# Kernel optimization log

Measured on AMD Instinct MI355X. Metric: run time of the kernel, lower is better.

Reference implementation:

```python
import jax, jax.numpy as jnp
import numpy as np

N, E, F, H, G = 50000, 800000, 128, 256, 64


def _bn(x, p, eps=1e-3):
    # inference-mode BatchNormalization; p rows = [gamma, beta, moving_mean, moving_var]
    g, b, m, v = p
    return g * (x - m) * jax.lax.rsqrt(v + eps) + b


def _prelu(x, a):
    return jnp.where(x >= 0, x, a * x)


def _dense_bn_act(x, W, b, bn, a=None):
    h = _bn(x @ W + b, bn)
    return h if a is None else _prelu(h, a)


def _gconv(x, src, tgt, W, b, bn, a, n_nodes):
    # spektral GeneralConv: Dense -> BN -> PReLU -> propagate (gather sources, scatter-sum to targets)
    h = _prelu(_bn(x @ W + b, bn), a)
    return jax.ops.segment_sum(h[src], tgt, num_segments=n_nodes)


def setup_inputs():
    key = jax.random.key(0)
    ks = iter(jax.random.split(key, 64))

    def dense(i, o):
        W = jax.random.normal(next(ks), (i, o), jnp.float32) / np.float32(np.sqrt(i))
        b = 0.01 * jax.random.normal(next(ks), (o,), jnp.float32)
        return W, b

    def bn_p(c):
        k1, k2, k3, k4 = jax.random.split(next(ks), 4)
        return jnp.stack([
            1.0 + 0.1 * jax.random.normal(k1, (c,)),
            0.1 * jax.random.normal(k2, (c,)),
            0.1 * jax.random.normal(k3, (c,)),
            0.5 + jax.random.uniform(k4, (c,)),
        ]).astype(jnp.float32)

    inp = {}
    inp['x'] = jax.random.normal(next(ks), (N, F), jnp.float32)
    inp['edge_index'] = jax.random.randint(next(ks), (E, 2), 0, N, jnp.int32)
    inp['seg'] = jnp.sort(jax.random.randint(next(ks), (N,), 0, G, jnp.int32))
    inp['n_graphs'] = G
    dims = {'pre0': F, 'pre1': H, 'g0': H, 'g1': 2 * H, 'g2': 3 * H, 'g3': 4 * H, 'post0': 5 * H}
    for name, din in dims.items():
        W, b = dense(din, H)
        inp[name + '_W'], inp[name + '_b'] = W, b
        inp[name + '_bn'] = bn_p(H)
        inp[name + '_a'] = jnp.full((H,), 0.25, jnp.float32)
    W, b = dense(H, 1)
    inp['post1_W'], inp['post1_b'] = W, b
    inp['post1_bn'] = bn_p(1)
    return inp


def reference(x, edge_index, seg, n_graphs, pre0_W, pre0_b, pre0_bn, pre0_a, pre1_W, pre1_b, pre1_bn, pre1_a, g0_W, g0_b, g0_bn, g0_a, g1_W, g1_b, g1_bn, g1_a, g2_W, g2_b, g2_bn, g2_a, g3_W, g3_b, g3_bn, g3_a, post0_W, post0_b, post0_bn, post0_a, post1_W, post1_b, post1_bn):
    n_nodes = x.shape[0]
    tgt, src = edge_index[:, 0], edge_index[:, 1]
    # pre-process MLP (2 layers)
    out = _dense_bn_act(x, pre0_W, pre0_b, pre0_bn, pre0_a)
    out = _dense_bn_act(out, pre1_W, pre1_b, pre1_bn, pre1_a)
    # 4 message-passing layers with 'cat' skip connectivity
    for W, b, bn, a in ((g0_W, g0_b, g0_bn, g0_a), (g1_W, g1_b, g1_bn, g1_a), (g2_W, g2_b, g2_bn, g2_a), (g3_W, g3_b, g3_bn, g3_a)):
        z = _gconv(out, src, tgt, W, b, bn, a, n_nodes)
        out = jnp.concatenate([z, out], axis=-1)
    # post-process MLP: hidden layer (PReLU) then linear output layer (BN, no activation)
    out = _dense_bn_act(out, post0_W, post0_b, post0_bn, post0_a)
    out = _dense_bn_act(out, post1_W, post1_b, post1_bn)
    # global sum pool over nodes per graph -> [n_graphs, 1]
    return jax.ops.segment_sum(out, seg, num_segments=n_graphs)
```

## Files before the change

kernel.cpp:

```cpp
#include <hip/hip_runtime.h>
#include <hip/hip_bf16.h>

#define NN 50000
#define NEDGE 800000
#define HD 256
#define ACT_LD 1280
#define NGRAPH 64
#define BN_EPS 1e-3f

#define BM 128
#define BN 128
#define BK 64

#define SCAN_NBLK ((NN + 255) / 256)

using bf16 = __hip_bfloat16;
typedef __attribute__((ext_vector_type(8))) short bf16x8;
typedef __attribute__((ext_vector_type(4))) float f32x4;

#define GLB(p) ((const __attribute__((address_space(1))) void*)(p))
#define LDS(p) ((__attribute__((address_space(3))) void*)(p))

static __device__ __forceinline__ float bf2f(unsigned short u) {
    union { float f; unsigned int i; } c;
    c.i = ((unsigned int)u) << 16;
    return c.f;
}
static __device__ __forceinline__ unsigned short f2bf(float f) {
    bf16 t = __float2bfloat16(f);
    return *reinterpret_cast<unsigned short*>(&t);
}

__global__ __launch_bounds__(256)
void transpose_w(const float* __restrict__ W, bf16* __restrict__ Wt, int K)
{
    __shared__ unsigned short T[32][33];
    const int k0 = blockIdx.x * 32;
    const int n0 = blockIdx.y * 32;
#pragma unroll
    for (int i = 0; i < 4; ++i) {
        const int idx = threadIdx.x + i * 256;
        const int kk = idx >> 5, nn = idx & 31;
        T[kk][nn] = f2bf(W[(size_t)(k0 + kk) * HD + n0 + nn]);
    }
    __syncthreads();
#pragma unroll
    for (int i = 0; i < 4; ++i) {
        const int idx = threadIdx.x + i * 256;
        const int nn = idx >> 5, kk = idx & 31;
        unsigned short v = T[kk][nn];
        Wt[(size_t)(n0 + nn) * K + k0 + kk] = *reinterpret_cast<bf16*>(&v);
    }
}

__global__ __launch_bounds__(256)
void convert_x(const float* __restrict__ x, bf16* __restrict__ xb)
{
    const int i = blockIdx.x * blockDim.x + threadIdx.x;
    if (i >= NN * 32) return;
    const float4 v = *reinterpret_cast<const float4*>(x + (size_t)i * 4);
    ushort4 o;
    o.x = f2bf(v.x); o.y = f2bf(v.y); o.z = f2bf(v.z); o.w = f2bf(v.w);
    *reinterpret_cast<ushort4*>((unsigned short*)xb + (size_t)i * 4) = o;
}

__global__ __launch_bounds__(256)
void gemm_bn_act(const bf16* __restrict__ A, int lda,
                 const bf16* __restrict__ Wt, int K,
                 const float* __restrict__ bias,
                 const float* __restrict__ bn,
                 const float* __restrict__ alpha,
                 bf16* __restrict__ out, int ldo, int M)
{
    __shared__ short As[BM * BK];
    __shared__ short Bs[BN * BK];

    const int tid  = threadIdx.x;
    const int wid  = tid >> 6;
    const int lane = tid & 63;
    const int lo   = lane & 15;
    const int hi   = lane >> 4;
    const int wr   = wid >> 1;
    const int wc   = wid & 1;

    const int m0 = blockIdx.x * BM;
    const int n0 = blockIdx.y * BN;

    const int srow = lane >> 3;
    const int sel  = (lane & 7) * 8;

    f32x4 acc[4][4] = {};

    for (int k0 = 0; k0 < K; k0 += BK) {
        __syncthreads();
#pragma unroll
        for (int i = 0; i < 4; ++i) {
            const int grp = wid * 4 + i;
            const int row = grp * 8 + srow;
            const int ar  = (m0 + row < M) ? (m0 + row) : (M - 1);
            __builtin_amdgcn_global_load_lds(GLB(A + (size_t)ar * lda + k0 + sel),
                                             LDS(&As[grp * 8 * BK]), 16, 0, 0);
            __builtin_amdgcn_global_load_lds(GLB(Wt + (size_t)(n0 + row) * K + k0 + sel),
                                             LDS(&Bs[grp * 8 * BK]), 16, 0, 0);
        }
        __syncthreads();

#pragma unroll
        for (int kc = 0; kc < 2; ++kc) {
            bf16x8 af[4], bfr[4];
#pragma unroll
            for (int rt = 0; rt < 4; ++rt)
                af[rt] = *reinterpret_cast<const bf16x8*>(&As[(wr * 64 + rt * 16 + lo) * BK + kc * 32 + hi * 8]);
#pragma unroll
            for (int ct = 0; ct < 4; ++ct)
                bfr[ct] = *reinterpret_cast<const bf16x8*>(&Bs[(wc * 64 + ct * 16 + lo) * BK + kc * 32 + hi * 8]);
#pragma unroll
            for (int rt = 0; rt < 4; ++rt)
#pragma unroll
                for (int ct = 0; ct < 4; ++ct)
                    acc[rt][ct] = __builtin_amdgcn_mfma_f32_16x16x32_bf16(af[rt], bfr[ct], acc[rt][ct], 0, 0, 0);
        }
    }

    float sc[4], sh[4], al[4];
#pragma unroll
    for (int ct = 0; ct < 4; ++ct) {
        const int c = n0 + wc * 64 + ct * 16 + lo;
        const float g  = bn[c];
        const float be = bn[HD + c];
        const float mu = bn[2 * HD + c];
        const float va = bn[3 * HD + c];
        sc[ct] = g * rsqrtf(va + BN_EPS);
        sh[ct] = be + (bias[c] - mu) * sc[ct];
        al[ct] = alpha ? alpha[c] : 1.0f;
    }
#pragma unroll
    for (int rt = 0; rt < 4; ++rt) {
#pragma unroll
        for (int i = 0; i < 4; ++i) {
            const int r = m0 + wr * 64 + rt * 16 + hi * 4 + i;
            if (r >= M) continue;
#pragma unroll
            for (int ct = 0; ct < 4; ++ct) {
                float v = acc[rt][ct][i] * sc[ct] + sh[ct];
                v = (v >= 0.f) ? v : al[ct] * v;
                unsigned short u = f2bf(v);
                out[(size_t)r * ldo + n0 + wc * 64 + ct * 16 + lo] = *reinterpret_cast<bf16*>(&u);
            }
        }
    }
}

__global__ __launch_bounds__(256)
void hist_tgt(const int* __restrict__ edge, int* __restrict__ ecnt)
{
    const int e = blockIdx.x * blockDim.x + threadIdx.x;
    if (e >= NEDGE) return;
    atomicAdd(&ecnt[edge[2 * e]], 1);
}

__global__ __launch_bounds__(256)
void block_sums(const int* __restrict__ ecnt, int* __restrict__ bsum)
{
    __shared__ int red[256];
    const int t = threadIdx.x;
    const int idx = blockIdx.x * 256 + t;
    red[t] = (idx < NN) ? ecnt[idx] : 0;
    __syncthreads();
#pragma unroll
    for (int d = 128; d > 0; d >>= 1) {
        if (t < d) red[t] += red[t + d];
        __syncthreads();
    }
    if (t == 0) bsum[blockIdx.x] = red[0];
}

__global__ __launch_bounds__(256)
void scan_bsums(const int* __restrict__ bsum, int* __restrict__ bbase,
                int* __restrict__ off)
{
    __shared__ int s[256];
    const int t = threadIdx.x;
    s[t] = (t < SCAN_NBLK) ? bsum[t] : 0;
    __syncthreads();
    for (int d = 1; d < 256; d <<= 1) {
        const int v = (t >= d) ? s[t - d] : 0;
        __syncthreads();
        s[t] += v;
        __syncthreads();
    }
    if (t < SCAN_NBLK) bbase[t] = (t == 0) ? 0 : s[t - 1];
    if (t == 255) off[NN] = s[255];
}

__global__ __launch_bounds__(256)
void block_scan(const int* __restrict__ ecnt, const int* __restrict__ bbase,
                int* __restrict__ off, int* __restrict__ cursor)
{
    __shared__ int s[256];
    const int t = threadIdx.x;
    const int idx = blockIdx.x * 256 + t;
    const int v = (idx < NN) ? ecnt[idx] : 0;
    s[t] = v;
    __syncthreads();
    for (int d = 1; d < 256; d <<= 1) {
        const int x = (t >= d) ? s[t - d] : 0;
        __syncthreads();
        s[t] += x;
        __syncthreads();
    }
    if (idx < NN) {
        const int excl = bbase[blockIdx.x] + s[t] - v;
        off[idx] = excl;
        cursor[idx] = excl;
    }
}

__global__ __launch_bounds__(256)
void fill_elist(const int* __restrict__ edge,
                int* __restrict__ cursor, int* __restrict__ elist)
{
    const int e = blockIdx.x * blockDim.x + threadIdx.x;
    if (e >= NEDGE) return;
    const int tgt = edge[2 * e + 0];
    const int src = edge[2 * e + 1];
    const int pos = atomicAdd(&cursor[tgt], 1);
    elist[pos] = src;
}

__global__ __launch_bounds__(256)
void gather_nodes(const bf16* __restrict__ h,
                  const int* __restrict__ off,
                  const int* __restrict__ elist,
                  bf16* __restrict__ dst)
{
    const int node = blockIdx.x * 4 + (threadIdx.x >> 6);
    if (node >= NN) return;
    const int lane = threadIdx.x & 63;
    const int j0 = off[node];
    const int j1 = off[node + 1];

    float4 a0 = make_float4(0.f, 0.f, 0.f, 0.f);
    float4 a1 = make_float4(0.f, 0.f, 0.f, 0.f);
    float4 a2 = make_float4(0.f, 0.f, 0.f, 0.f);
    float4 a3 = make_float4(0.f, 0.f, 0.f, 0.f);

    int j = j0;
    for (; j + 4 <= j1; j += 4) {
        const int s0 = elist[j + 0];
        const int s1 = elist[j + 1];
        const int s2 = elist[j + 2];
        const int s3 = elist[j + 3];
        const ushort4 u0 = *reinterpret_cast<const ushort4*>(h + (size_t)s0 * HD + lane * 4);
        const ushort4 u1 = *reinterpret_cast<const ushort4*>(h + (size_t)s1 * HD + lane * 4);
        const ushort4 u2 = *reinterpret_cast<const ushort4*>(h + (size_t)s2 * HD + lane * 4);
        const ushort4 u3 = *reinterpret_cast<const ushort4*>(h + (size_t)s3 * HD + lane * 4);
        a0.x += bf2f(u0.x); a0.y += bf2f(u0.y); a0.z += bf2f(u0.z); a0.w += bf2f(u0.w);
        a1.x += bf2f(u1.x); a1.y += bf2f(u1.y); a1.z += bf2f(u1.z); a1.w += bf2f(u1.w);
        a2.x += bf2f(u2.x); a2.y += bf2f(u2.y); a2.z += bf2f(u2.z); a2.w += bf2f(u2.w);
        a3.x += bf2f(u3.x); a3.y += bf2f(u3.y); a3.z += bf2f(u3.z); a3.w += bf2f(u3.w);
    }
    for (; j < j1; ++j) {
        const int s0 = elist[j];
        const ushort4 u0 = *reinterpret_cast<const ushort4*>(h + (size_t)s0 * HD + lane * 4);
        a0.x += bf2f(u0.x); a0.y += bf2f(u0.y); a0.z += bf2f(u0.z); a0.w += bf2f(u0.w);
    }

    const float rx = (a0.x + a1.x) + (a2.x + a3.x);
    const float ry = (a0.y + a1.y) + (a2.y + a3.y);
    const float rz = (a0.z + a1.z) + (a2.z + a3.z);
    const float rw = (a0.w + a1.w) + (a2.w + a3.w);

    ushort4 o;
    o.x = f2bf(rx); o.y = f2bf(ry); o.z = f2bf(rz); o.w = f2bf(rw);
    *reinterpret_cast<ushort4*>(dst + (size_t)node * ACT_LD + lane * 4) = o;
}

__global__ __launch_bounds__(256)
void post1_segsum(const bf16* __restrict__ h,
                  const float* __restrict__ W,
                  const float* __restrict__ b,
                  const float* __restrict__ bn,
                  const int* __restrict__ seg,
                  float* __restrict__ outg)
{
    __shared__ float bins[NGRAPH];
    const int t = threadIdx.x;
    if (t < NGRAPH) bins[t] = 0.f;
    __syncthreads();

    const int wave = t >> 6;
    const int lane = t & 63;
    const float4 wv = *reinterpret_cast<const float4*>(W + lane * 4);
    const float g = bn[0], be = bn[1], mu = bn[2], va = bn[3];
    const float bscale = g * rsqrtf(va + BN_EPS);
    const float b0 = b[0];

    const int row0 = blockIdx.x * 64 + wave * 16;
#pragma unroll
    for (int i = 0; i < 16; ++i) {
        const int row = row0 + i;
        if (row >= NN) break;
        const ushort4 u = *reinterpret_cast<const ushort4*>(h + (size_t)row * HD + lane * 4);
        float s = bf2f(u.x) * wv.x + bf2f(u.y) * wv.y + bf2f(u.z) * wv.z + bf2f(u.w) * wv.w;
#pragma unroll
        for (int off = 32; off > 0; off >>= 1) s += __shfl_down(s, off);
        if (lane == 0) {
            const float y = bscale * (s + b0 - mu) + be;
            atomicAdd(&bins[seg[row]], y);
        }
    }
    __syncthreads();
    if (t < NGRAPH && bins[t] != 0.f) atomicAdd(&outg[t], bins[t]);
}

extern "C" void kernel_launch(void* const* d_in, const int* in_sizes, int n_in,
                              void* d_out, int out_size, void* d_ws, size_t ws_size,
                              hipStream_t stream)
{
    const float* x    = (const float*)d_in[0];
    const int*   edge = (const int*)d_in[1];
    const int*   seg  = (const int*)d_in[2];

    const float* Wsrc[7], *bi[7], *bnp[7], *ap[7];
    for (int L = 0; L < 7; ++L) {
        Wsrc[L] = (const float*)d_in[4 + 4 * L + 0];
        bi[L]   = (const float*)d_in[4 + 4 * L + 1];
        bnp[L]  = (const float*)d_in[4 + 4 * L + 2];
        ap[L]   = (const float*)d_in[4 + 4 * L + 3];
    }
    const float* post1_W  = (const float*)d_in[32];
    const float* post1_b  = (const float*)d_in[33];
    const float* post1_bn = (const float*)d_in[34];

    static const int Ks[7] = {128, 256, 256, 512, 768, 1024, 1280};

    bf16* act  = (bf16*)d_ws;
    bf16* h    = act + (size_t)NN * ACT_LD;
    bf16* xb   = h + (size_t)NN * HD;
    bf16* wt0  = xb + (size_t)NN * 128;
    bf16* WtB[7];
    {
        size_t o = 0;
        for (int L = 0; L < 7; ++L) { WtB[L] = wt0 + o; o += (size_t)Ks[L] * HD; }
    }
    int* ecnt   = (int*)(wt0 + (size_t)4224 * HD);
    int* off    = ecnt + NN;
    int* cursor = off + NN + 1;
    int* elist  = cursor + NN;
    int* bsum   = elist + NEDGE;
    int* bbase  = bsum + SCAN_NBLK;

    hipMemsetAsync(d_out, 0, (size_t)out_size * sizeof(float), stream);
    hipMemsetAsync(ecnt, 0, NN * sizeof(int), stream);

    const dim3 blk(256);
    const dim3 gemm_grid((NN + BM - 1) / BM, HD / BN);
    const int  edge_grid = (NEDGE + 255) / 256;
    const int  node_grid = (NN + 3) / 4;

    for (int L = 0; L < 7; ++L)
        transpose_w<<<dim3(Ks[L] / 32, HD / 32), blk, 0, stream>>>(Wsrc[L], WtB[L], Ks[L]);
    convert_x<<<(NN * 32 + 255) / 256, blk, 0, stream>>>(x, xb);

    hist_tgt<<<edge_grid, blk, 0, stream>>>(edge, ecnt);
    block_sums<<<SCAN_NBLK, blk, 0, stream>>>(ecnt, bsum);
    scan_bsums<<<1, blk, 0, stream>>>(bsum, bbase, off);
    block_scan<<<SCAN_NBLK, blk, 0, stream>>>(ecnt, bbase, off, cursor);
    fill_elist<<<edge_grid, blk, 0, stream>>>(edge, cursor, elist);

    gemm_bn_act<<<gemm_grid, blk, 0, stream>>>(xb, 128, WtB[0], 128, bi[0], bnp[0], ap[0], h, HD, NN);
    gemm_bn_act<<<gemm_grid, blk, 0, stream>>>(h, HD, WtB[1], 256, bi[1], bnp[1], ap[1], act + 1024, ACT_LD, NN);

    for (int L = 0; L < 4; ++L) {
        const int in_off = 1024 - 256 * L;
        const int K      = 256 * (L + 1);
        gemm_bn_act<<<gemm_grid, blk, 0, stream>>>(act + in_off, ACT_LD, WtB[2 + L], K, bi[2 + L], bnp[2 + L], ap[2 + L], h, HD, NN);
        gather_nodes<<<node_grid, blk, 0, stream>>>(h, off, elist, act + (in_off - 256));
    }

    gemm_bn_act<<<gemm_grid, blk, 0, stream>>>(act, ACT_LD, WtB[6], 1280, bi[6], bnp[6], ap[6], h, HD, NN);
    post1_segsum<<<(NN + 63) / 64, blk, 0, stream>>>(h, post1_W, post1_b, post1_bn, seg, (float*)d_out);
}
```

Before: 618.0 us.

## Double-buffer GEMM LDS tiles and XOR-swizzle LDS layout

The GEMM now keeps two LDS buffers, so global-to-LDS loads for the next K tile are issued before computing the current tile. Explicit vmcnt waits and barriers replace the old pair of __syncthreads per iteration. The LDS layout is also XOR-swizzled by row to avoid bank conflicts on the MFMA fragment reads. LDS use doubles, which may lower occupancy, and correctness depends on the hand-written wait counts.

Measured after the change: 711.1 us. 1.15x slower.

```diff
diff --git a/kernel.cpp b/kernel.cpp
--- a/kernel.cpp
+++ b/kernel.cpp
@@ -72,8 +72,10 @@
                  const float* __restrict__ alpha,
                  bf16* __restrict__ out, int ldo, int M)
 {
-    __shared__ short As[BM * BK];
-    __shared__ short Bs[BN * BK];
+    __shared__ short As0[BM * BK];
+    __shared__ short Bs0[BN * BK];
+    __shared__ short As1[BM * BK];
+    __shared__ short Bs1[BN * BK];
 
     const int tid  = threadIdx.x;
     const int wid  = tid >> 6;
@@ -87,40 +89,80 @@
     const int n0 = blockIdx.y * BN;
 
     const int srow = lane >> 3;
-    const int sel  = (lane & 7) * 8;
+    const int ssel = ((lane & 7) ^ srow) * 8;
+
+    const int nt = K / BK;
 
     f32x4 acc[4][4] = {};
 
-    for (int k0 = 0; k0 < K; k0 += BK) {
-        __syncthreads();
-#pragma unroll
-        for (int i = 0; i < 4; ++i) {
-            const int grp = wid * 4 + i;
-            const int row = grp * 8 + srow;
-            const int ar  = (m0 + row < M) ? (m0 + row) : (M - 1);
-            __builtin_amdgcn_global_load_lds(GLB(A + (size_t)ar * lda + k0 + sel),
-                                             LDS(&As[grp * 8 * BK]), 16, 0, 0);
-            __builtin_amdgcn_global_load_lds(GLB(Wt + (size_t)(n0 + row) * K + k0 + sel),
-                                             LDS(&Bs[grp * 8 * BK]), 16, 0, 0);
+#define STAGE_T(BUFA, BUFB, kt) do {                                                     \
+    const int kk0 = (kt) * BK;                                                           \
+    _Pragma("unroll")                                                                    \
+    for (int i_ = 0; i_ < 4; ++i_) {                                                     \
+        const int grp = wid * 4 + i_;                                                    \
+        const int row = grp * 8 + srow;                                                  \
+        const int ar  = (m0 + row < M) ? (m0 + row) : (M - 1);                           \
+        __builtin_amdgcn_global_load_lds(GLB(A + (size_t)ar * lda + kk0 + ssel),         \
+                                         LDS(&BUFA[grp * 8 * BK]), 16, 0, 0);            \
+        __builtin_amdgcn_global_load_lds(GLB(Wt + (size_t)(n0 + row) * K + kk0 + ssel),  \
+                                         LDS(&BUFB[grp * 8 * BK]), 16, 0, 0);            \
+    } } while (0)
+
+#define COMPUTE_T(BUFA, BUFB) do {                                                       \
+    _Pragma("unroll")                                                                    \
+    for (int kc = 0; kc < 2; ++kc) {                                                     \
+        bf16x8 af[4], bfr[4];                                                            \
+        _Pragma("unroll")                                                                \
+        for (int rt = 0; rt < 4; ++rt) {                                                 \
+            const int row = wr * 64 + rt * 16 + lo;                                      \
+            const int ch  = (kc * 4 + hi) ^ (row & 7);                                   \
+            af[rt] = *reinterpret_cast<const bf16x8*>(&BUFA[row * BK + ch * 8]);         \
+        }                                                                                \
+        _Pragma("unroll")                                                                \
+        for (int ct = 0; ct < 4; ++ct) {                                                 \
+            const int rowb = wc * 64 + ct * 16 + lo;                                     \
+            const int chb  = (kc * 4 + hi) ^ (rowb & 7);                                 \
+            bfr[ct] = *reinterpret_cast<const bf16x8*>(&BUFB[rowb * BK + chb * 8]);      \
+        }                                                                                \
+        _Pragma("unroll")                                                                \
+        for (int rt = 0; rt < 4; ++rt)                                                   \
+            _Pragma("unroll")                                                            \
+            for (int ct = 0; ct < 4; ++ct)                                               \
+                acc[rt][ct] = __builtin_amdgcn_mfma_f32_16x16x32_bf16(af[rt], bfr[ct],   \
+                                                                     acc[rt][ct], 0, 0, 0); \
+    } } while (0)
+
+    STAGE_T(As0, Bs0, 0);
+    int t = 0;
+    while (t < nt) {
+        if (t + 1 < nt) {
+            STAGE_T(As1, Bs1, t + 1);
+            asm volatile("s_waitcnt vmcnt(8)" ::: "memory");
+        } else {
+            asm volatile("s_waitcnt vmcnt(0)" ::: "memory");
         }
-        __syncthreads();
-
-#pragma unroll
-        for (int kc = 0; kc < 2; ++kc) {
-            bf16x8 af[4], bfr[4];
-#pragma unroll
-            for (int rt = 0; rt < 4; ++rt)
-                af[rt] = *reinterpret_cast<const bf16x8*>(&As[(wr * 64 + rt * 16 + lo) * BK + kc * 32 + hi * 8]);
-#pragma unroll
-            for (int ct = 0; ct < 4; ++ct)
-                bfr[ct] = *reinterpret_cast<const bf16x8*>(&Bs[(wc * 64 + ct * 16 + lo) * BK + kc * 32 + hi * 8]);
-#pragma unroll
-            for (int rt = 0; rt < 4; ++rt)
-#pragma unroll
-                for (int ct = 0; ct < 4; ++ct)
-                    acc[rt][ct] = __builtin_amdgcn_mfma_f32_16x16x32_bf16(af[rt], bfr[ct], acc[rt][ct], 0, 0, 0);
+        __builtin_amdgcn_s_barrier();
+        __builtin_amdgcn_sched_barrier(0);
+        COMPUTE_T(As0, Bs0);
+        __builtin_amdgcn_s_barrier();
+        __builtin_amdgcn_sched_barrier(0);
+        ++t;
+        if (t >= nt) break;
+        if (t + 1 < nt) {
+            STAGE_T(As0, Bs0, t + 1);
+            asm volatile("s_waitcnt vmcnt(8)" ::: "memory");
+        } else {
+            asm volatile("s_waitcnt vmcnt(0)" ::: "memory");
         }
-    }
+        __builtin_amdgcn_s_barrier();
+        __builtin_amdgcn_sched_barrier(0);
+        COMPUTE_T(As1, Bs1);
+        __builtin_amdgcn_s_barrier();
+        __builtin_amdgcn_sched_barrier(0);
+        ++t;
+    }
+#undef STAGE_T
+#undef COMPUTE_T
 
     float sc[4], sh[4], al[4];
 #pragma unroll
```
